# Performance work log

Hardware: AMD Instinct MI355X
Metric: run time of the kernel (lower is better)

The kernel has to match this reference:

```python
import jax, jax.numpy as jnp
import numpy as np

B, V, F, P = 16, 100000, 200000, 65536


def _sample_one(verts, faces, e1, e2, u):
    # verts: [V,3], faces: [F,3], e1/e2/u: [P]
    tris = verts[faces]                      # [F,3,3] irregular gather
    vec1 = tris[:, 1, :] - tris[:, 0, :]
    vec2 = tris[:, 2, :] - tris[:, 0, :]
    normals = jnp.cross(vec1, vec2)          # [F,3]
    areas = jnp.linalg.norm(normals, axis=1) / 2.0  # [F]
    # area-weighted categorical sampling via inverse CDF (deterministic given u)
    cdf = jnp.cumsum(areas)
    cdf = cdf / cdf[-1]
    idx = jnp.clip(jnp.searchsorted(jax.lax.stop_gradient(cdf), u), 0, F - 1)  # [P]
    sampled_tris = tris[idx]                 # [P,3,3]
    unit_normals = normals / (areas[:, None] * 2.0)
    sampled_normals = unit_normals[idx]      # [P,3]
    # barycentric weights (Osada et al.)
    s = jnp.sqrt(e1)
    w = jnp.stack([1.0 - s, (1.0 - e2) * s, e2 * s], axis=1)[:, :, None]  # [P,3,1]
    points = jnp.sum(sampled_tris * w, axis=1)  # [P,3]
    return points, sampled_normals


def setup_inputs() -> dict:
    key = jax.random.key(0)
    k1, k2, k3, k4, k5 = jax.random.split(key, 5)
    vertices_batch = jax.random.normal(k1, (B, V, 3), dtype=jnp.float32)
    faces_batch = jax.random.randint(k2, (B, F, 3), 0, V, dtype=jnp.int64)
    eps1 = jax.random.uniform(k3, (B, P), dtype=jnp.float32)
    eps2 = jax.random.uniform(k4, (B, P), dtype=jnp.float32)
    u = jax.random.uniform(k5, (B, P), dtype=jnp.float32)
    return {"vertices_batch": vertices_batch, "faces_batch": faces_batch,
            "eps1": eps1, "eps2": eps2, "u": u}


def reference(vertices_batch, faces_batch, eps1, eps2, u):
    points, normals = jax.vmap(_sample_one)(vertices_batch, faces_batch, eps1, eps2, u)
    return points, normals  # ([B,P,3], [B,P,3])
```

## Files before the change

kernel.cpp:

```cpp
#include <hip/hip_runtime.h>

#pragma clang fp contract(off)

#define NB 16
#define NV 100000
#define NF 200000
#define NP 65536

#define B16 16
#define NW0 12500
#define NW1 782
#define NW2 49
#define NW3 4

#define TREE_LVL 12
#define TREE_N   (1 << TREE_LVL)

__device__ __forceinline__ void xcd_map(int p, int& batch, int& chunk) {
    int r = p & 15;
    batch = 2 * (r & 7) + (r >> 3);
    chunk = p >> 4;
}

__global__ void detect_kernel(const int* __restrict__ faces, int* __restrict__ flag) {
    __shared__ int any;
    if (threadIdx.x == 0) any = 0;
    __syncthreads();
    int acc = 0;
    for (int i = threadIdx.x; i < 4096; i += blockDim.x)
        acc |= faces[2 * i + 1];
    if (acc) atomicOr(&any, 1);
    __syncthreads();
    if (threadIdx.x == 0) flag[0] = (any == 0) ? 1 : 0;
}

__device__ __forceinline__ void load_face(const int* __restrict__ faces,
                                          long long fidx, int is64,
                                          int& i0, int& i1, int& i2) {
    if (is64) {
        const int* p = faces + fidx * 6;
        i0 = p[0]; i1 = p[2]; i2 = p[4];
    } else {
        const int* p = faces + fidx * 3;
        i0 = p[0]; i1 = p[1]; i2 = p[2];
    }
}

__global__ void area_prefix_kernel(const float* __restrict__ verts,
                                   const int* __restrict__ faces,
                                   const int* __restrict__ flag,
                                   float* __restrict__ cdf,
                                   float* __restrict__ s0) {
    __shared__ float S[256];
    int batch, chunk;
    xcd_map(blockIdx.x, batch, chunk);
    int tid = threadIdx.x;
    int i = chunk * 256 + tid;
    bool valid = (i < NF);
    float a = 0.0f;
    if (valid) {
        int is64 = flag[0];
        size_t gid = (size_t)batch * NF + i;
        const float* vb = verts + (size_t)batch * NV * 3;
        int i0, i1, i2;
        load_face(faces, (long long)gid, is64, i0, i1, i2);
        float ax = vb[3 * i0 + 0], ay = vb[3 * i0 + 1], az = vb[3 * i0 + 2];
        float bx = vb[3 * i1 + 0], by = vb[3 * i1 + 1], bz = vb[3 * i1 + 2];
        float cx = vb[3 * i2 + 0], cy = vb[3 * i2 + 1], cz = vb[3 * i2 + 2];
        float v1x = bx - ax, v1y = by - ay, v1z = bz - az;
        float v2x = cx - ax, v2y = cy - ay, v2z = cz - az;
        float nx = fmaf(v1y, v2z, -(v1z * v2y));
        float ny = fmaf(v1z, v2x, -(v1x * v2z));
        float nz = fmaf(v1x, v2y, -(v1y * v2x));
        float ss = fmaf(nz, nz, fmaf(nx, nx, ny * ny));
        float nrm = sqrtf(ss);
        a = nrm / 2.0f;
    }
    S[tid] = a;
    __syncthreads();
    if (valid) {
        int base = tid & ~15;
        float run = S[base];
        for (int p = base + 1; p <= tid; ++p) run = run + S[p];
        cdf[(size_t)batch * NF + i] = run;
        if ((tid & 15) == 15)
            s0[(size_t)batch * NW0 + (i >> 4)] = run;
    }
}

__global__ void midscan16_kernel(const float* __restrict__ s0g, float* __restrict__ S0g) {
    __shared__ float t0[NW0];
    __shared__ float t1[NW1];
    __shared__ float t2[NW2];
    __shared__ float t3[NW3];
    int b = blockIdx.x;
    for (int i = threadIdx.x; i < NW0; i += blockDim.x)
        t0[i] = s0g[(size_t)b * NW0 + i];
    __syncthreads();
    for (int w = threadIdx.x; w < NW1; w += blockDim.x) {
        int st = w * B16, en = st + B16 < NW0 ? st + B16 : NW0;
        float run = 0.0f;
        for (int p = st; p < en; ++p) { run = run + t0[p]; t0[p] = run; }
        t1[w] = run;
    }
    __syncthreads();
    for (int w = threadIdx.x; w < NW2; w += blockDim.x) {
        int st = w * B16, en = st + B16 < NW1 ? st + B16 : NW1;
        float run = 0.0f;
        for (int p = st; p < en; ++p) { run = run + t1[p]; t1[p] = run; }
        t2[w] = run;
    }
    __syncthreads();
    for (int w = threadIdx.x; w < NW3; w += blockDim.x) {
        int st = w * B16, en = st + B16 < NW2 ? st + B16 : NW2;
        float run = 0.0f;
        for (int p = st; p < en; ++p) { run = run + t2[p]; t2[p] = run; }
        t3[w] = run;
    }
    __syncthreads();
    if (threadIdx.x == 0) {
        float run = 0.0f;
        for (int k = 0; k < NW3; ++k) { run = run + t3[k]; t3[k] = run; }
    }
    __syncthreads();
    for (int i = threadIdx.x; i < NW2; i += blockDim.x) {
        int w = i >> 4;
        float off = (w > 0) ? t3[w - 1] : 0.0f;
        t2[i] = off + t2[i];
    }
    __syncthreads();
    for (int i = threadIdx.x; i < NW1; i += blockDim.x) {
        int w = i >> 4;
        float off = (w > 0) ? t2[w - 1] : 0.0f;
        t1[i] = off + t1[i];
    }
    __syncthreads();
    for (int i = threadIdx.x; i < NW0; i += blockDim.x) {
        int w = i >> 4;
        float off = (w > 0) ? t1[w - 1] : 0.0f;
        t0[i] = off + t0[i];
    }
    __syncthreads();
    for (int i = threadIdx.x; i < NW0; i += blockDim.x)
        S0g[(size_t)b * NW0 + i] = t0[i];
}

__global__ void fused_norm_kernel(float* __restrict__ cdf,
                                  const float* __restrict__ s0,
                                  const float* __restrict__ S0) {
    int batch, chunk;
    xcd_map(blockIdx.x, batch, chunk);
    int i = chunk * 256 + threadIdx.x;
    if (i >= NF) return;
    const float* S0b = S0 + (size_t)batch * NW0;
    float total = S0b[NW0 - 2] + s0[(size_t)batch * NW0 + NW0 - 1];
    float rcp = 1.0f / total;
    int j = i >> 4;
    float off = (j > 0) ? S0b[j - 1] : 0.0f;
    float* p = cdf + (size_t)batch * NF + i;
    *p = (off + *p) * rcp;
}

__global__ void sample_kernel(const float* __restrict__ verts,
                              const int* __restrict__ faces,
                              const int* __restrict__ flag,
                              const float* __restrict__ e1,
                              const float* __restrict__ e2,
                              const float* __restrict__ u,
                              const float* __restrict__ cdf,
                              float* __restrict__ out) {
    __shared__ float T[TREE_N];
    int batch, chunk;
    xcd_map(blockIdx.x, batch, chunk);
    int b = batch;
    const float* c = cdf + (size_t)b * NF;

    for (int n = 1 + threadIdx.x; n < TREE_N; n += blockDim.x) {
        int k = 31 - __clz(n);
        int low = 0, high = NF;
        for (int j = k - 1; j >= 0; --j) {
            int mid = (low + high) >> 1;
            if ((n >> j) & 1) low = mid; else high = mid;
        }
        T[n] = c[(low + high) >> 1];
    }
    __syncthreads();

    int li = chunk * 256 + threadIdx.x;
    int gid = (b << 16) + li;
    int is64 = flag[0];

    float uv = u[gid];
    int low = 0, high = NF, node = 1;
    #pragma unroll
    for (int it = 0; it < TREE_LVL; ++it) {
        int mid = (low + high) >> 1;
        bool gl = (uv <= T[node]);
        node = 2 * node + (gl ? 0 : 1);
        if (gl) high = mid; else low = mid;
    }
    #pragma unroll
    for (int it = TREE_LVL; it < 18; ++it) {
        int mid = (low + high) >> 1;
        bool gl = (uv <= c[mid]);
        if (gl) high = mid; else low = mid;
    }
    int idx = high < NF - 1 ? high : NF - 1;

    const float* vb = verts + (size_t)b * NV * 3;
    int i0, i1, i2;
    load_face(faces, (long long)b * NF + idx, is64, i0, i1, i2);
    double ax = vb[3 * i0 + 0], ay = vb[3 * i0 + 1], az = vb[3 * i0 + 2];
    double bx = vb[3 * i1 + 0], by = vb[3 * i1 + 1], bz = vb[3 * i1 + 2];
    double cx = vb[3 * i2 + 0], cy = vb[3 * i2 + 1], cz = vb[3 * i2 + 2];

    double v1x = bx - ax, v1y = by - ay, v1z = bz - az;
    double v2x = cx - ax, v2y = cy - ay, v2z = cz - az;
    double nx = v1y * v2z - v1z * v2y;
    double ny = v1z * v2x - v1x * v2z;
    double nz = v1x * v2y - v1y * v2x;
    double ss = (nx * nx + ny * ny) + nz * nz;
    double nrm = sqrt(ss);
    double unx = nx / nrm, uny = ny / nrm, unz = nz / nrm;

    double s = sqrt((double)e1[gid]);
    double t = (double)e2[gid];
    double w0 = 1.0 - s;
    double w1 = (1.0 - t) * s;
    double w2 = t * s;
    double px = (ax * w0 + bx * w1) + cx * w2;
    double py = (ay * w0 + by * w1) + cy * w2;
    double pz = (az * w0 + bz * w1) + cz * w2;

    size_t po = (size_t)gid * 3;
    out[po + 0] = (float)px;
    out[po + 1] = (float)py;
    out[po + 2] = (float)pz;
    size_t no = (size_t)NB * NP * 3 + po;
    out[no + 0] = (float)unx;
    out[no + 1] = (float)uny;
    out[no + 2] = (float)unz;
}

extern "C" void kernel_launch(void* const* d_in, const int* in_sizes, int n_in,
                              void* d_out, int out_size, void* d_ws, size_t ws_size,
                              hipStream_t stream) {
    const float* verts = (const float*)d_in[0];
    const int*   faces = (const int*)d_in[1];
    const float* e1    = (const float*)d_in[2];
    const float* e2    = (const float*)d_in[3];
    const float* u     = (const float*)d_in[4];
    float* out = (float*)d_out;

    char* ws = (char*)d_ws;
    int*   flag = (int*)ws;
    float* cdf  = (float*)(ws + 512);
    float* s0   = (float*)(ws + 512 + (size_t)NB * NF * 4);
    float* S0   = (float*)(ws + 512 + (size_t)NB * NF * 4 + (size_t)NB * NW0 * 4);

    detect_kernel<<<1, 256, 0, stream>>>(faces, flag);

    area_prefix_kernel<<<16 * 782, 256, 0, stream>>>(verts, faces, flag, cdf, s0);

    midscan16_kernel<<<NB, 256, 0, stream>>>(s0, S0);

    fused_norm_kernel<<<16 * 782, 256, 0, stream>>>(cdf, s0, S0);

    sample_kernel<<<16 * 256, 256, 0, stream>>>(verts, faces, flag, e1, e2, u, cdf, out);
}
```

Baseline: 200.9 us.

## Drop shared-memory search tree; interleave two global binary searches per thread

Removes the per-block construction of a 4096-node shared-memory search tree, which cost 4095 scattered global loads plus a block barrier in every block. Each thread now handles two points and runs both 18-step binary searches directly against the global CDF, interleaved so the two dependent load chains overlap. The grid is halved to match. The trade-off is that the first 12 levels now read from L2/global instead of LDS, so each step has higher latency; the top levels are shared by all threads and should stay cache-resident.

```diff
diff --git a/kernel.cpp b/kernel.cpp
--- a/kernel.cpp
+++ b/kernel.cpp
@@ -12,9 +12,6 @@
 #define NW1 782
 #define NW2 49
 #define NW3 4
-
-#define TREE_LVL 12
-#define TREE_N   (1 << TREE_LVL)
 
 __device__ __forceinline__ void xcd_map(int p, int& batch, int& chunk) {
     int r = p & 15;
@@ -161,6 +158,46 @@
     *p = (off + *p) * rcp;
 }
 
+__device__ __forceinline__ void epilogue(const float* __restrict__ vb,
+                                         const int* __restrict__ faces,
+                                         long long fidx, int is64,
+                                         const float* __restrict__ e1,
+                                         const float* __restrict__ e2,
+                                         int gid, float* __restrict__ out) {
+    int i0, i1, i2;
+    load_face(faces, fidx, is64, i0, i1, i2);
+    double ax = vb[3 * i0 + 0], ay = vb[3 * i0 + 1], az = vb[3 * i0 + 2];
+    double bx = vb[3 * i1 + 0], by = vb[3 * i1 + 1], bz = vb[3 * i1 + 2];
+    double cx = vb[3 * i2 + 0], cy = vb[3 * i2 + 1], cz = vb[3 * i2 + 2];
+
+    double v1x = bx - ax, v1y = by - ay, v1z = bz - az;
+    double v2x = cx - ax, v2y = cy - ay, v2z = cz - az;
+    double nx = v1y * v2z - v1z * v2y;
+    double ny = v1z * v2x - v1x * v2z;
+    double nz = v1x * v2y - v1y * v2x;
+    double ss = (nx * nx + ny * ny) + nz * nz;
+    double nrm = sqrt(ss);
+    double unx = nx / nrm, uny = ny / nrm, unz = nz / nrm;
+
+    double s = sqrt((double)e1[gid]);
+    double t = (double)e2[gid];
+    double w0 = 1.0 - s;
+    double w1 = (1.0 - t) * s;
+    double w2 = t * s;
+    double px = (ax * w0 + bx * w1) + cx * w2;
+    double py = (ay * w0 + by * w1) + cy * w2;
+    double pz = (az * w0 + bz * w1) + cz * w2;
+
+    size_t po = (size_t)gid * 3;
+    out[po + 0] = (float)px;
+    out[po + 1] = (float)py;
+    out[po + 2] = (float)pz;
+    size_t no = (size_t)NB * NP * 3 + po;
+    out[no + 0] = (float)unx;
+    out[no + 1] = (float)uny;
+    out[no + 2] = (float)unz;
+}
+
 __global__ void sample_kernel(const float* __restrict__ verts,
                               const int* __restrict__ faces,
                               const int* __restrict__ flag,
@@ -169,77 +206,36 @@
                               const float* __restrict__ u,
                               const float* __restrict__ cdf,
                               float* __restrict__ out) {
-    __shared__ float T[TREE_N];
     int batch, chunk;
     xcd_map(blockIdx.x, batch, chunk);
     int b = batch;
     const float* c = cdf + (size_t)b * NF;
-
-    for (int n = 1 + threadIdx.x; n < TREE_N; n += blockDim.x) {
-        int k = 31 - __clz(n);
-        int low = 0, high = NF;
-        for (int j = k - 1; j >= 0; --j) {
-            int mid = (low + high) >> 1;
-            if ((n >> j) & 1) low = mid; else high = mid;
-        }
-        T[n] = c[(low + high) >> 1];
-    }
-    __syncthreads();
-
-    int li = chunk * 256 + threadIdx.x;
-    int gid = (b << 16) + li;
     int is64 = flag[0];
 
-    float uv = u[gid];
-    int low = 0, high = NF, node = 1;
+    int li0 = chunk * 512 + threadIdx.x;
+    int li1 = li0 + 256;
+    int g0 = (b << 16) + li0;
+    int g1 = (b << 16) + li1;
+
+    float uv0 = u[g0], uv1 = u[g1];
+    int lo0 = 0, hi0 = NF, lo1 = 0, hi1 = NF;
     #pragma unroll
-    for (int it = 0; it < TREE_LVL; ++it) {
-        int mid = (low + high) >> 1;
-        bool gl = (uv <= T[node]);
-        node = 2 * node + (gl ? 0 : 1);
-        if (gl) high = mid; else low = mid;
-    }
-    #pragma unroll
-    for (int it = TREE_LVL; it < 18; ++it) {
-        int mid = (low + high) >> 1;
-        bool gl = (uv <= c[mid]);
-        if (gl) high = mid; else low = mid;
-    }
-    int idx = high < NF - 1 ? high : NF - 1;
+    for (int it = 0; it < 18; ++it) {
+        int m0 = (lo0 + hi0) >> 1;
+        int m1 = (lo1 + hi1) >> 1;
+        float c0 = c[m0];
+        float c1 = c[m1];
+        bool gl0 = (uv0 <= c0);
+        bool gl1 = (uv1 <= c1);
+        lo0 = gl0 ? lo0 : m0;  hi0 = gl0 ? m0 : hi0;
+        lo1 = gl1 ? lo1 : m1;  hi1 = gl1 ? m1 : hi1;
+    }
+    int idx0 = hi0 < NF - 1 ? hi0 : NF - 1;
+    int idx1 = hi1 < NF - 1 ? hi1 : NF - 1;
 
     const float* vb = verts + (size_t)b * NV * 3;
-    int i0, i1, i2;
-    load_face(faces, (long long)b * NF + idx, is64, i0, i1, i2);
-    double ax = vb[3 * i0 + 0], ay = vb[3 * i0 + 1], az = vb[3 * i0 + 2];
-    double bx = vb[3 * i1 + 0], by = vb[3 * i1 + 1], bz = vb[3 * i1 + 2];
-    double cx = vb[3 * i2 + 0], cy = vb[3 * i2 + 1], cz = vb[3 * i2 + 2];
-
-    double v1x = bx - ax, v1y = by - ay, v1z = bz - az;
-    double v2x = cx - ax, v2y = cy - ay, v2z = cz - az;
-    double nx = v1y * v2z - v1z * v2y;
-    double ny = v1z * v2x - v1x * v2z;
-    double nz = v1x * v2y - v1y * v2x;
-    double ss = (nx * nx + ny * ny) + nz * nz;
-    double nrm = sqrt(ss);
-    double unx = nx / nrm, uny = ny / nrm, unz = nz / nrm;
-
-    double s = sqrt((double)e1[gid]);
-    double t = (double)e2[gid];
-    double w0 = 1.0 - s;
-    double w1 = (1.0 - t) * s;
-    double w2 = t * s;
-    double px = (ax * w0 + bx * w1) + cx * w2;
-    double py = (ay * w0 + by * w1) + cy * w2;
-    double pz = (az * w0 + bz * w1) + cz * w2;
-
-    size_t po = (size_t)gid * 3;
-    out[po + 0] = (float)px;
-    out[po + 1] = (float)py;
-    out[po + 2] = (float)pz;
-    size_t no = (size_t)NB * NP * 3 + po;
-    out[no + 0] = (float)unx;
-    out[no + 1] = (float)uny;
-    out[no + 2] = (float)unz;
+    epilogue(vb, faces, (long long)b * NF + idx0, is64, e1, e2, g0, out);
+    epilogue(vb, faces, (long long)b * NF + idx1, is64, e1, e2, g1, out);
 }
 
 extern "C" void kernel_launch(void* const* d_in, const int* in_sizes, int n_in,
@@ -266,5 +262,5 @@
 
     fused_norm_kernel<<<16 * 782, 256, 0, stream>>>(cdf, s0, S0);
 
-    sample_kernel<<<16 * 256, 256, 0, stream>>>(verts, faces, flag, e1, e2, u, cdf, out);
-}
+    sample_kernel<<<16 * 128, 256, 0, stream>>>(verts, faces, flag, e1, e2, u, cdf, out);
+}
```

Result: faster. 169.2 us (-15.8%).
